# Kernel tuning notes

Hardware: AMD Instinct MI355X
Metric: run time of the kernel (lower is better)

The kernel has to match this reference:

```python
import jax, jax.numpy as jnp
import numpy as np

N, E, F, C, H, L, ED = 100000, 1600000, 128, 16, 2, 2, 4
EPS = 1e-5
NEG_SLOPE = 0.2


def setup_inputs() -> dict:
    key = jax.random.key(0)
    ks = jax.random.split(key, 32)
    s = 0.1
    inp = {
        "x": jax.random.normal(ks[0], (N, F), dtype=jnp.float32),
        "edge_index": jax.random.randint(ks[1], (2, E), 0, N, dtype=jnp.int64),
        "edge_attr": jax.random.uniform(ks[2], (E, ED), dtype=jnp.float32),
        "embed_W": jax.random.normal(ks[3], (F, C)) * s,
        "embed_b": jnp.zeros((C,), jnp.float32),
        "ln0_w": jnp.ones((C,), jnp.float32),
        "ln0_b": jnp.zeros((C,), jnp.float32),
        "Wl": jax.random.normal(ks[4], (L, C, H * C)) * s,
        "bl": jnp.zeros((L, H * C), jnp.float32),
        "Wr": jax.random.normal(ks[5], (L, C, H * C)) * s,
        "br": jnp.zeros((L, H * C), jnp.float32),
        "We": jax.random.normal(ks[6], (L, ED, H * C)) * s,
        "att": jax.random.normal(ks[7], (L, H, C)) * s,
        "gat_b": jnp.zeros((L, H * C), jnp.float32),
        "n1_w": jnp.ones((L, H * C), jnp.float32),
        "n1_b": jnp.zeros((L, H * C), jnp.float32),
        "lin_W": jax.random.normal(ks[8], (L, H * C, C)) * s,
        "lin_b": jnp.zeros((L, C), jnp.float32),
        "n2_w": jnp.ones((L, C), jnp.float32),
        "n2_b": jnp.zeros((L, C), jnp.float32),
    }
    return inp


def _node_ln(v, w, b):
    # torch.nn.LayerNorm over the feature dim (per node)
    mu = v.mean(-1, keepdims=True)
    var = ((v - mu) ** 2).mean(-1, keepdims=True)
    return (v - mu) / jnp.sqrt(var + EPS) * w + b


def _graph_ln(v, w, b):
    # PyG norm.LayerNorm(mode='graph'): normalize over ALL nodes and channels
    mu = v.mean()
    vc = v - mu
    return vc / jnp.sqrt((vc * vc).mean() + EPS) * w + b


def reference(x, edge_index, edge_attr, embed_W, embed_b, ln0_w, ln0_b,
              Wl, bl, Wr, br, We, att, gat_b, n1_w, n1_b,
              lin_W, lin_b, n2_w, n2_b):
    n = x.shape[0]
    heads, c = att.shape[1], att.shape[2]
    layers = Wl.shape[0]

    # node embedding MLP (dropout = identity in eval)
    h = jax.nn.relu(_node_ln(x @ embed_W + embed_b, ln0_w, ln0_b))

    # add self-loops (fill_value=0.0 -> zero edge features, lin_edge has no bias)
    loop = jnp.arange(n)
    src = jnp.concatenate([edge_index[0], loop])
    dst = jnp.concatenate([edge_index[1], loop])

    hs = [h]
    for i in range(layers):
        xl = (h @ Wl[i] + bl[i]).reshape(n, heads, c)   # source transform (x_j)
        xr = (h @ Wr[i] + br[i]).reshape(n, heads, c)   # target transform (x_i)
        ew = (edge_attr @ We[i]).reshape(-1, heads, c)
        ew = jnp.concatenate([ew, jnp.zeros((n, heads, c), ew.dtype)], axis=0)

        msg = xl[src] + xr[dst] + ew                      # [E+N, H, C]
        logits = jnp.einsum('ehc,hc->eh', jax.nn.leaky_relu(msg, NEG_SLOPE), att[i])
        m = jax.ops.segment_max(logits, dst, num_segments=n)
        ex = jnp.exp(logits - m[dst])
        den = jax.ops.segment_sum(ex, dst, num_segments=n)
        alpha = ex / den[dst]                             # segment softmax over dst

        g = jax.ops.segment_sum(alpha[..., None] * xl[src], dst, num_segments=n)
        g = g.reshape(n, heads * c) + gat_b[i]

        g = jax.nn.relu(_graph_ln(g, n1_w[i], n1_b[i]))
        g = g @ lin_W[i] + lin_b[i]
        g = _graph_ln(g, n2_w[i], n2_b[i])
        h = jax.nn.relu(g + h)                            # residual + relu
        hs.append(h)

    # JumpingKnowledge mode='max': elementwise max over layer outputs
    return jnp.max(jnp.stack(hs, axis=0), axis=0)
```

## Files before the change

kernel.cpp:

```cpp
#include <hip/hip_runtime.h>

#define N_NODES 100000
#define N_EDGES 1600000
#define NF 128
#define NC 16
#define NH 2
#define HC 32
#define NL 2
#define NED 4
#define EPS 1e-5f
#define NEG 0.2f
#define NBUCK 196
#define P1_CHUNK 4096
#define P1_BLKS ((N_EDGES + P1_CHUNK - 1) / P1_CHUNK)
#define AGG_BLKS ((N_NODES + 7) / 8)
#define MID_BLKS ((N_NODES + 15) / 16)

__device__ __forceinline__ unsigned short f2bf(float f) {
    unsigned int u = __float_as_uint(f);
    u += 0x7fffu + ((u >> 16) & 1u);
    return (unsigned short)(u >> 16);
}
__device__ __forceinline__ float bf2f(unsigned short u) {
    return __uint_as_float(((unsigned int)u) << 16);
}

__global__ __launch_bounds__(256) void k_embed(
    const float* __restrict__ x, const float* __restrict__ W,
    const float* __restrict__ b, const float* __restrict__ lnw,
    const float* __restrict__ lnb, float* __restrict__ h, float* __restrict__ jk)
{
    __shared__ float Ws[NF * NC];
    __shared__ float xs[16][NF + 4];
    const int t = threadIdx.x;
    for (int i = t; i < NF * NC; i += 256) Ws[i] = W[i];
    const int n0 = blockIdx.x * 16;
    for (int i = t; i < 16 * NF; i += 256) {
        int r = i >> 7, f = i & (NF - 1);
        int n = n0 + r;
        xs[r][f] = (n < N_NODES) ? x[(size_t)n * NF + f] : 0.f;
    }
    __syncthreads();
    const int r = t >> 4;
    const int c = t & 15;
    const int n = n0 + r;
    float acc = b[c];
#pragma unroll 16
    for (int f = 0; f < NF; ++f) acc += xs[r][f] * Ws[f * NC + c];
    float s = acc;
    for (int m = 8; m >= 1; m >>= 1) s += __shfl_xor(s, m, 16);
    float mu = s * (1.f / 16.f);
    float d = acc - mu;
    float v = d * d;
    for (int m = 8; m >= 1; m >>= 1) v += __shfl_xor(v, m, 16);
    float inv = rsqrtf(v * (1.f / 16.f) + EPS);
    float out = fmaxf(d * inv * lnw[c] + lnb[c], 0.f);
    if (n < N_NODES) {
        h[(size_t)n * NC + c]  = out;
        jk[(size_t)n * NC + c] = out;
    }
}

__global__ __launch_bounds__(256) void k_bhist(
    const int* __restrict__ dst, int* __restrict__ bcnt)
{
    __shared__ int hist[256];
    const int t = threadIdx.x;
    hist[t] = 0;
    __syncthreads();
    const int e0 = blockIdx.x * P1_CHUNK;
    const int cnt = min(P1_CHUNK, N_EDGES - e0);
    for (int i = t; i < cnt; i += 256)
        atomicAdd(&hist[dst[e0 + i] >> 9], 1);
    __syncthreads();
    if (hist[t] > 0) atomicAdd(&bcnt[t], hist[t]);
}

__global__ __launch_bounds__(256) void k_bscan(
    const int* __restrict__ bcnt, int* __restrict__ bbase, int* __restrict__ bcur)
{
    __shared__ int tmp[256];
    const int t = threadIdx.x;
    int v0 = bcnt[t];
    tmp[t] = v0;
    __syncthreads();
    for (int off = 1; off < 256; off <<= 1) {
        int v = (t >= off) ? tmp[t - off] : 0;
        __syncthreads();
        tmp[t] += v;
        __syncthreads();
    }
    int excl = tmp[t] - v0;
    bbase[t] = excl;
    bcur[t]  = excl;
    if (t == 255) bbase[256] = tmp[t];
}

__global__ __launch_bounds__(256) void k_pass1(
    const int* __restrict__ src, const int* __restrict__ dst,
    int* __restrict__ bcur, int2* __restrict__ csr_tmp)
{
    __shared__ int2 stage[P1_CHUNK];
    __shared__ unsigned char bstage[P1_CHUNK];
    __shared__ int hist[256];
    __shared__ int exc[256];
    __shared__ int gbase[256];
    __shared__ int scanbuf[256];
    const int t = threadIdx.x;
    const int e0 = blockIdx.x * P1_CHUNK;
    const int cnt = min(P1_CHUNK, N_EDGES - e0);
    hist[t] = 0;
    __syncthreads();
    int mys[16], myb[16], myp[16];
    int nv = 0;
#pragma unroll
    for (int k = 0; k < 16; ++k) {
        int i = k * 256 + t;
        if (i < cnt) {
            int e = e0 + i;
            int d = dst[e];
            mys[nv] = src[e];
            myb[nv] = d >> 9;
            myp[nv] = (e << 9) | (d & 511);
            atomicAdd(&hist[d >> 9], 1);
            ++nv;
        }
    }
    __syncthreads();
    int hv = hist[t];
    scanbuf[t] = hv;
    __syncthreads();
    for (int off = 1; off < 256; off <<= 1) {
        int v = (t >= off) ? scanbuf[t - off] : 0;
        __syncthreads();
        scanbuf[t] += v;
        __syncthreads();
    }
    int ex = scanbuf[t] - hv;
    hist[t] = ex;
    exc[t]  = ex;
    __syncthreads();
    for (int k = 0; k < nv; ++k) {
        int pos = atomicAdd(&hist[myb[k]], 1);
        stage[pos]  = make_int2(mys[k], myp[k]);
        bstage[pos] = (unsigned char)myb[k];
    }
    __syncthreads();
    {
        int c = hist[t] - exc[t];
        gbase[t] = (c > 0) ? atomicAdd(&bcur[t], c) : 0;
    }
    __syncthreads();
    for (int i = t; i < cnt; i += 256) {
        int b = bstage[i];
        csr_tmp[gbase[b] + (i - exc[b])] = stage[i];
    }
}

__global__ __launch_bounds__(256) void k_pass2(
    const int* __restrict__ bbase, const int2* __restrict__ csr_tmp,
    int* __restrict__ offsets, int2* __restrict__ csr_se)
{
    __shared__ int hist[512];
    __shared__ int cur[512];
    __shared__ int scanbuf[256];
    const int b = blockIdx.x, t = threadIdx.x;
    const int ebeg = bbase[b], eend = bbase[b + 1];
    hist[t] = 0; hist[t + 256] = 0;
    __syncthreads();
    for (int i = ebeg + t; i < eend; i += 256)
        atomicAdd(&hist[csr_tmp[i].y & 511], 1);
    __syncthreads();
    int a0 = hist[2 * t], a1 = hist[2 * t + 1];
    int pair = a0 + a1;
    scanbuf[t] = pair;
    __syncthreads();
    for (int off = 1; off < 256; off <<= 1) {
        int v = (t >= off) ? scanbuf[t - off] : 0;
        __syncthreads();
        scanbuf[t] += v;
        __syncthreads();
    }
    int e2 = scanbuf[t] - pair;
    cur[2 * t]     = e2;
    cur[2 * t + 1] = e2 + a0;
    __syncthreads();
    const int n0 = b * 512;
#pragma unroll
    for (int k = 0; k < 2; ++k) {
        int i = t + k * 256;
        int n = n0 + i;
        if (n < N_NODES) offsets[n] = ebeg + cur[i];
    }
    if (b == NBUCK - 1 && t == 0) offsets[N_NODES] = N_EDGES;
    __syncthreads();
    for (int i = ebeg + t; i < eend; i += 256) {
        int2 se = csr_tmp[i];
        int dl = se.y & 511;
        int e  = (int)(((unsigned int)se.y) >> 9);
        int pos = ebeg + atomicAdd(&cur[dl], 1);
        csr_se[pos] = make_int2(se.x, e);
    }
}

__global__ __launch_bounds__(256) void k_trans(
    const float* __restrict__ h, const float* __restrict__ Wl, const float* __restrict__ bl,
    const float* __restrict__ Wr, const float* __restrict__ br,
    unsigned short* __restrict__ xl, unsigned short* __restrict__ xr)
{
    __shared__ float Wls[NC * HC], Wrs[NC * HC];
    __shared__ float hs[8][NC + 1];
    const int t = threadIdx.x;
    for (int i = t; i < NC * HC; i += 256) { Wls[i] = Wl[i]; Wrs[i] = Wr[i]; }
    const int n0 = blockIdx.x * 8;
    for (int i = t; i < 8 * NC; i += 256) {
        int r = i >> 4, c = i & 15;
        int n = n0 + r;
        hs[r][c] = (n < N_NODES) ? h[(size_t)n * NC + c] : 0.f;
    }
    __syncthreads();
    const int r = t >> 5;
    const int j = t & 31;
    const int n = n0 + r;
    float al = bl[j], ar = br[j];
#pragma unroll
    for (int c = 0; c < NC; ++c) {
        float hv = hs[r][c];
        al += hv * Wls[c * HC + j];
        ar += hv * Wrs[c * HC + j];
    }
    if (n < N_NODES) {
        xl[(size_t)n * HC + j] = f2bf(al);
        xr[(size_t)n * HC + j] = f2bf(ar);
    }
}

__device__ __forceinline__ float head_sum(float p) {
    p += __shfl_xor(p, 1, 16);
    p += __shfl_xor(p, 2, 16);
    p += __shfl_xor(p, 4, 16);
    p += __shfl_xor(p, 8, 16);
    return p;
}

__global__ __launch_bounds__(256) void k_agg(
    const int* __restrict__ offsets, const int2* __restrict__ csr_se,
    const float4* __restrict__ ea4,
    const float* __restrict__ We, const float* __restrict__ att,
    const float* __restrict__ gat_b,
    const unsigned short* __restrict__ xl, const unsigned short* __restrict__ xr,
    float* __restrict__ g, float2* __restrict__ part)
{
    __shared__ float Wes[NED * HC];
    __shared__ float atts[HC], gbs[HC];
    const int t = threadIdx.x;
    if (t < NED * HC) Wes[t] = We[t];
    if (t < HC) { atts[t] = att[t]; gbs[t] = gat_b[t]; }
    __syncthreads();
    const int grp = t >> 5;
    const int j   = t & 31;
    const int d = blockIdx.x * 8 + grp;
    float gv = 0.f;
    if (d < N_NODES) {
        const float aj = atts[j];
        const float w0 = Wes[j], w1 = Wes[HC + j], w2 = Wes[2 * HC + j], w3 = Wes[3 * HC + j];
        const float xld = bf2f(xl[(size_t)d * HC + j]);
        const float xrd = bf2f(xr[(size_t)d * HC + j]);
        float m = xld + xrd;
        m = (m > 0.f) ? m : NEG * m;
        float eh = __expf(head_sum(m * aj));
        float acc = eh * xld;
        float den = eh;
        const int base = offsets[d];
        const int deg  = offsets[d + 1] - base;
        int k = 0;
        for (; k + 4 <= deg; k += 4) {
            const int2 s0 = csr_se[base + k];
            const int2 s1 = csr_se[base + k + 1];
            const int2 s2 = csr_se[base + k + 2];
            const int2 s3 = csr_se[base + k + 3];
            const float x0 = bf2f(xl[(size_t)s0.x * HC + j]);
            const float x1 = bf2f(xl[(size_t)s1.x * HC + j]);
            const float x2 = bf2f(xl[(size_t)s2.x * HC + j]);
            const float x3 = bf2f(xl[(size_t)s3.x * HC + j]);
            const float4 e0 = ea4[s0.y];
            const float4 e1 = ea4[s1.y];
            const float4 e2 = ea4[s2.y];
            const float4 e3 = ea4[s3.y];
            float m0 = x0 + xrd + e0.x * w0 + e0.y * w1 + e0.z * w2 + e0.w * w3;
            float m1 = x1 + xrd + e1.x * w0 + e1.y * w1 + e1.z * w2 + e1.w * w3;
            float m2 = x2 + xrd + e2.x * w0 + e2.y * w1 + e2.z * w2 + e2.w * w3;
            float m3 = x3 + xrd + e3.x * w0 + e3.y * w1 + e3.z * w2 + e3.w * w3;
            m0 = (m0 > 0.f) ? m0 : NEG * m0;
            m1 = (m1 > 0.f) ? m1 : NEG * m1;
            m2 = (m2 > 0.f) ? m2 : NEG * m2;
            m3 = (m3 > 0.f) ? m3 : NEG * m3;
            float p0 = m0 * aj, p1 = m1 * aj, p2 = m2 * aj, p3 = m3 * aj;
            p0 += __shfl_xor(p0, 1, 16); p1 += __shfl_xor(p1, 1, 16);
            p2 += __shfl_xor(p2, 1, 16); p3 += __shfl_xor(p3, 1, 16);
            p0 += __shfl_xor(p0, 2, 16); p1 += __shfl_xor(p1, 2, 16);
            p2 += __shfl_xor(p2, 2, 16); p3 += __shfl_xor(p3, 2, 16);
            p0 += __shfl_xor(p0, 4, 16); p1 += __shfl_xor(p1, 4, 16);
            p2 += __shfl_xor(p2, 4, 16); p3 += __shfl_xor(p3, 4, 16);
            p0 += __shfl_xor(p0, 8, 16); p1 += __shfl_xor(p1, 8, 16);
            p2 += __shfl_xor(p2, 8, 16); p3 += __shfl_xor(p3, 8, 16);
            const float ee0 = __expf(p0), ee1 = __expf(p1);
            const float ee2 = __expf(p2), ee3 = __expf(p3);
            acc += ee0 * x0 + ee1 * x1 + ee2 * x2 + ee3 * x3;
            den += ee0 + ee1 + ee2 + ee3;
        }
        for (; k < deg; ++k) {
            const int2 se = csr_se[base + k];
            const float xv = bf2f(xl[(size_t)se.x * HC + j]);
            const float4 ea = ea4[se.y];
            float mm = xv + xrd + ea.x * w0 + ea.y * w1 + ea.z * w2 + ea.w * w3;
            mm = (mm > 0.f) ? mm : NEG * mm;
            const float ee = __expf(head_sum(mm * aj));
            acc += ee * xv;
            den += ee;
        }
        gv = acc / den + gbs[j];
        g[(size_t)d * HC + j] = gv;
    }
    float s = gv, ss = gv * gv;
    for (int m = 32; m >= 1; m >>= 1) { s += __shfl_xor(s, m); ss += __shfl_xor(ss, m); }
    __shared__ float sr[4], ssr[4];
    const int w = t >> 6;
    if ((t & 63) == 0) { sr[w] = s; ssr[w] = ss; }
    __syncthreads();
    if (t == 0) part[blockIdx.x] = make_float2(sr[0] + sr[1] + sr[2] + sr[3],
                                               ssr[0] + ssr[1] + ssr[2] + ssr[3]);
}

__global__ __launch_bounds__(256) void k_red(
    const float2* __restrict__ part, int n, double* __restrict__ out)
{
    const int t = threadIdx.x;
    double s = 0.0, ss = 0.0;
    for (int i = t; i < n; i += 256) {
        float2 p = part[i];
        s += (double)p.x; ss += (double)p.y;
    }
    for (int m = 32; m >= 1; m >>= 1) { s += __shfl_xor(s, m); ss += __shfl_xor(ss, m); }
    __shared__ double sr[4], ssr[4];
    const int w = t >> 6;
    if ((t & 63) == 0) { sr[w] = s; ssr[w] = ss; }
    __syncthreads();
    if (t == 0) {
        out[0] = sr[0] + sr[1] + sr[2] + sr[3];
        out[1] = ssr[0] + ssr[1] + ssr[2] + ssr[3];
    }
}

__global__ __launch_bounds__(256) void k_mid(
    const float* __restrict__ g,
    const float* __restrict__ n1w, const float* __restrict__ n1b,
    const float* __restrict__ linW, const float* __restrict__ linb,
    const double* __restrict__ stats1, float* __restrict__ g2,
    float2* __restrict__ part)
{
    __shared__ float Ws[HC * NC];
    __shared__ float rs[16][HC + 1];
    const int t = threadIdx.x;
    for (int i = t; i < HC * NC; i += 256) Ws[i] = linW[i];
    const double cnt = (double)N_NODES * HC;
    const double mud = stats1[0] / cnt;
    const float mu  = (float)mud;
    const float var = (float)(stats1[1] / cnt - mud * mud);
    const float inv = rsqrtf(var + EPS);
    const int n0 = blockIdx.x * 16;
    for (int i = t; i < 16 * HC; i += 256) {
        int r = i >> 5, j = i & 31;
        int n = n0 + r;
        float v = (n < N_NODES) ? g[(size_t)n * HC + j] : mu;
        v = (v - mu) * inv * n1w[j] + n1b[j];
        rs[r][j] = fmaxf(v, 0.f);
    }
    __syncthreads();
    const int r = t >> 4, c = t & 15;
    const int n = n0 + r;
    float acc = linb[c];
#pragma unroll
    for (int j = 0; j < HC; ++j) acc += rs[r][j] * Ws[j * NC + c];
    float val = (n < N_NODES) ? acc : 0.f;
    if (n < N_NODES) g2[(size_t)n * NC + c] = acc;
    float s = val, ss = val * val;
    for (int m = 32; m >= 1; m >>= 1) { s += __shfl_xor(s, m); ss += __shfl_xor(ss, m); }
    __shared__ float sr[4], ssr[4];
    const int w = t >> 6;
    if ((t & 63) == 0) { sr[w] = s; ssr[w] = ss; }
    __syncthreads();
    if (t == 0) part[blockIdx.x] = make_float2(sr[0] + sr[1] + sr[2] + sr[3],
                                               ssr[0] + ssr[1] + ssr[2] + ssr[3]);
}

__global__ __launch_bounds__(256) void k_final(
    const float* __restrict__ g2, const float* __restrict__ n2w,
    const float* __restrict__ n2b, const double* __restrict__ stats2,
    float* __restrict__ h, float* __restrict__ jk)
{
    const int i = blockIdx.x * 256 + threadIdx.x;
    if (i >= N_NODES * NC) return;
    const double cnt = (double)N_NODES * NC;
    const double mud = stats2[0] / cnt;
    const float mu  = (float)mud;
    const float var = (float)(stats2[1] / cnt - mud * mud);
    const float inv = rsqrtf(var + EPS);
    const int c = i & (NC - 1);
    float v = (g2[i] - mu) * inv * n2w[c] + n2b[c];
    float hn = fmaxf(v + h[i], 0.f);
    h[i] = hn;
    jk[i] = fmaxf(jk[i], hn);
}

extern "C" void kernel_launch(void* const* d_in, const int* in_sizes, int n_in,
                              void* d_out, int out_size, void* d_ws, size_t ws_size,
                              hipStream_t stream)
{
    const float* x     = (const float*)d_in[0];
    const int*   eidx  = (const int*)d_in[1];
    const float* eattr = (const float*)d_in[2];
    const float* embW  = (const float*)d_in[3];
    const float* embB  = (const float*)d_in[4];
    const float* ln0w  = (const float*)d_in[5];
    const float* ln0b  = (const float*)d_in[6];
    const float* Wl    = (const float*)d_in[7];
    const float* bl    = (const float*)d_in[8];
    const float* Wr    = (const float*)d_in[9];
    const float* br    = (const float*)d_in[10];
    const float* We    = (const float*)d_in[11];
    const float* att   = (const float*)d_in[12];
    const float* gatb  = (const float*)d_in[13];
    const float* n1w   = (const float*)d_in[14];
    const float* n1b   = (const float*)d_in[15];
    const float* linW  = (const float*)d_in[16];
    const float* linb  = (const float*)d_in[17];
    const float* n2w   = (const float*)d_in[18];
    const float* n2b   = (const float*)d_in[19];
    float* out = (float*)d_out;

    char* ws = (char*)d_ws;
    double* stats = (double*)ws;
    char* p = ws + 1024;
    int* bcnt  = (int*)p;  p += 1024;
    int* bbase = (int*)p;  p += 2048;
    int* bcur  = (int*)p;  p += 1024;
    int* offsets = (int*)p; p += (size_t)(N_NODES + 64) * 4;
    int2* csr_tmp = (int2*)p; p += (size_t)N_EDGES * 8;
    int2* csr_se  = (int2*)p; p += (size_t)N_EDGES * 8;
    float* h  = (float*)p;   p += (size_t)N_NODES * NC * 4;
    unsigned short* xl = (unsigned short*)p; p += (size_t)N_NODES * HC * 2;
    unsigned short* xr = (unsigned short*)p; p += (size_t)N_NODES * HC * 2;
    float* g   = (float*)p;  p += (size_t)N_NODES * HC * 4;
    float* g2  = (float*)p;  p += (size_t)N_NODES * NC * 4;
    float2* part1 = (float2*)p; p += (size_t)AGG_BLKS * 8;
    float2* part2 = (float2*)p; p += (size_t)MID_BLKS * 8;

    const int* srcp = eidx;
    const int* dstp = eidx + N_EDGES;

    hipMemsetAsync(bcnt, 0, 1024, stream);
    k_bhist<<<P1_BLKS, 256, 0, stream>>>(dstp, bcnt);
    k_bscan<<<1, 256, 0, stream>>>(bcnt, bbase, bcur);
    k_pass1<<<P1_BLKS, 256, 0, stream>>>(srcp, dstp, bcur, csr_tmp);
    k_pass2<<<NBUCK, 256, 0, stream>>>(bbase, csr_tmp, offsets, csr_se);

    k_embed<<<(N_NODES + 15) / 16, 256, 0, stream>>>(x, embW, embB, ln0w, ln0b, h, out);

    for (int l = 0; l < NL; ++l) {
        k_trans<<<(N_NODES + 7) / 8, 256, 0, stream>>>(
            h, Wl + l * NC * HC, bl + l * HC, Wr + l * NC * HC, br + l * HC, xl, xr);
        k_agg<<<AGG_BLKS, 256, 0, stream>>>(
            offsets, csr_se, (const float4*)eattr, We + l * NED * HC, att + l * HC,
            gatb + l * HC, xl, xr, g, part1);
        k_red<<<1, 256, 0, stream>>>(part1, AGG_BLKS, stats);
        k_mid<<<MID_BLKS, 256, 0, stream>>>(
            g, n1w + l * HC, n1b + l * HC,
            linW + l * HC * NC, linb + l * NC, stats, g2, part2);
        k_red<<<1, 256, 0, stream>>>(part2, MID_BLKS, stats + 2);
        k_final<<<(N_NODES * NC + 255) / 256, 256, 0, stream>>>(
            g2, n2w + l * NC, n2b + l * NC, stats + 2, h, out);
    }
}
```

Before: 516.3 us.

## Permute edge attributes into CSR order and fuse reductions via last-block pattern

```diff
diff --git a/kernel.cpp b/kernel.cpp
--- a/kernel.cpp
+++ b/kernel.cpp
@@ -62,9 +62,11 @@
 }
 
 __global__ __launch_bounds__(256) void k_bhist(
-    const int* __restrict__ dst, int* __restrict__ bcnt)
+    const int* __restrict__ dst, int* __restrict__ bcnt, unsigned* __restrict__ ctr,
+    int* __restrict__ bbase, int* __restrict__ bcur)
 {
     __shared__ int hist[256];
+    __shared__ bool amLast;
     const int t = threadIdx.x;
     hist[t] = 0;
     __syncthreads();
@@ -74,31 +76,35 @@
         atomicAdd(&hist[dst[e0 + i] >> 9], 1);
     __syncthreads();
     if (hist[t] > 0) atomicAdd(&bcnt[t], hist[t]);
-}
-
-__global__ __launch_bounds__(256) void k_bscan(
-    const int* __restrict__ bcnt, int* __restrict__ bbase, int* __restrict__ bcur)
-{
-    __shared__ int tmp[256];
-    const int t = threadIdx.x;
-    int v0 = bcnt[t];
-    tmp[t] = v0;
-    __syncthreads();
-    for (int off = 1; off < 256; off <<= 1) {
-        int v = (t >= off) ? tmp[t - off] : 0;
-        __syncthreads();
-        tmp[t] += v;
-        __syncthreads();
-    }
-    int excl = tmp[t] - v0;
-    bbase[t] = excl;
-    bcur[t]  = excl;
-    if (t == 255) bbase[256] = tmp[t];
+    __syncthreads();
+    if (t == 0) {
+        __threadfence();
+        amLast = (atomicAdd(ctr, 1u) == (unsigned)gridDim.x - 1u);
+    }
+    __syncthreads();
+    if (amLast) {
+        __threadfence();
+        int v0 = ((volatile int*)bcnt)[t];
+        __shared__ int tmp[256];
+        tmp[t] = v0;
+        __syncthreads();
+        for (int off = 1; off < 256; off <<= 1) {
+            int v = (t >= off) ? tmp[t - off] : 0;
+            __syncthreads();
+            tmp[t] += v;
+            __syncthreads();
+        }
+        int excl = tmp[t] - v0;
+        bbase[t] = excl;
+        bcur[t]  = excl;
+        if (t == 255) bbase[256] = tmp[t];
+    }
 }
 
 __global__ __launch_bounds__(256) void k_pass1(
     const int* __restrict__ src, const int* __restrict__ dst,
-    int* __restrict__ bcur, int2* __restrict__ csr_tmp)
+    const float4* __restrict__ ea4, int* __restrict__ bcur,
+    int2* __restrict__ tmp_se, float4* __restrict__ tmp_ea)
 {
     __shared__ int2 stage[P1_CHUNK];
     __shared__ unsigned char bstage[P1_CHUNK];
@@ -153,13 +159,18 @@
     __syncthreads();
     for (int i = t; i < cnt; i += 256) {
         int b = bstage[i];
-        csr_tmp[gbase[b] + (i - exc[b])] = stage[i];
+        int2 se = stage[i];
+        int e = (int)(((unsigned int)se.y) >> 9);
+        int gpos = gbase[b] + (i - exc[b]);
+        tmp_se[gpos] = se;
+        tmp_ea[gpos] = ea4[e];
     }
 }
 
 __global__ __launch_bounds__(256) void k_pass2(
-    const int* __restrict__ bbase, const int2* __restrict__ csr_tmp,
-    int* __restrict__ offsets, int2* __restrict__ csr_se)
+    const int* __restrict__ bbase, const int2* __restrict__ tmp_se,
+    const float4* __restrict__ tmp_ea,
+    int* __restrict__ offsets, int* __restrict__ csr_src, float4* __restrict__ csr_ea)
 {
     __shared__ int hist[512];
     __shared__ int cur[512];
@@ -169,7 +180,7 @@
     hist[t] = 0; hist[t + 256] = 0;
     __syncthreads();
     for (int i = ebeg + t; i < eend; i += 256)
-        atomicAdd(&hist[csr_tmp[i].y & 511], 1);
+        atomicAdd(&hist[tmp_se[i].y & 511], 1);
     __syncthreads();
     int a0 = hist[2 * t], a1 = hist[2 * t + 1];
     int pair = a0 + a1;
@@ -181,9 +192,9 @@
         scanbuf[t] += v;
         __syncthreads();
     }
-    int e2 = scanbuf[t] - pair;
-    cur[2 * t]     = e2;
-    cur[2 * t + 1] = e2 + a0;
+    int ex2 = scanbuf[t] - pair;
+    cur[2 * t]     = ex2;
+    cur[2 * t + 1] = ex2 + a0;
     __syncthreads();
     const int n0 = b * 512;
 #pragma unroll
@@ -195,11 +206,12 @@
     if (b == NBUCK - 1 && t == 0) offsets[N_NODES] = N_EDGES;
     __syncthreads();
     for (int i = ebeg + t; i < eend; i += 256) {
-        int2 se = csr_tmp[i];
+        int2 se = tmp_se[i];
+        float4 ea = tmp_ea[i];
         int dl = se.y & 511;
-        int e  = (int)(((unsigned int)se.y) >> 9);
         int pos = ebeg + atomicAdd(&cur[dl], 1);
-        csr_se[pos] = make_int2(se.x, e);
+        csr_src[pos] = se.x;
+        csr_ea[pos]  = ea;
     }
 }
 
@@ -244,15 +256,17 @@
 }
 
 __global__ __launch_bounds__(256) void k_agg(
-    const int* __restrict__ offsets, const int2* __restrict__ csr_se,
-    const float4* __restrict__ ea4,
+    const int* __restrict__ offsets, const int* __restrict__ csr_src,
+    const float4* __restrict__ csr_ea,
     const float* __restrict__ We, const float* __restrict__ att,
     const float* __restrict__ gat_b,
     const unsigned short* __restrict__ xl, const unsigned short* __restrict__ xr,
-    float* __restrict__ g, float2* __restrict__ part)
+    float* __restrict__ g, float2* __restrict__ part,
+    unsigned* __restrict__ ctr, double* __restrict__ stats)
 {
     __shared__ float Wes[NED * HC];
     __shared__ float atts[HC], gbs[HC];
+    __shared__ bool amLast;
     const int t = threadIdx.x;
     if (t < NED * HC) Wes[t] = We[t];
     if (t < HC) { atts[t] = att[t]; gbs[t] = gat_b[t]; }
@@ -275,18 +289,15 @@
         const int deg  = offsets[d + 1] - base;
         int k = 0;
         for (; k + 4 <= deg; k += 4) {
-            const int2 s0 = csr_se[base + k];
-            const int2 s1 = csr_se[base + k + 1];
-            const int2 s2 = csr_se[base + k + 2];
-            const int2 s3 = csr_se[base + k + 3];
-            const float x0 = bf2f(xl[(size_t)s0.x * HC + j]);
-            const float x1 = bf2f(xl[(size_t)s1.x * HC + j]);
-            const float x2 = bf2f(xl[(size_t)s2.x * HC + j]);
-            const float x3 = bf2f(xl[(size_t)s3.x * HC + j]);
-            const float4 e0 = ea4[s0.y];
-            const float4 e1 = ea4[s1.y];
-            const float4 e2 = ea4[s2.y];
-            const float4 e3 = ea4[s3.y];
+            const int b0 = base + k;
+            const int s0 = csr_src[b0],     s1 = csr_src[b0 + 1];
+            const int s2 = csr_src[b0 + 2], s3 = csr_src[b0 + 3];
+            const float4 e0 = csr_ea[b0],     e1 = csr_ea[b0 + 1];
+            const float4 e2 = csr_ea[b0 + 2], e3 = csr_ea[b0 + 3];
+            const float x0 = bf2f(xl[(size_t)s0 * HC + j]);
+            const float x1 = bf2f(xl[(size_t)s1 * HC + j]);
+            const float x2 = bf2f(xl[(size_t)s2 * HC + j]);
+            const float x3 = bf2f(xl[(size_t)s3 * HC + j]);
             float m0 = x0 + xrd + e0.x * w0 + e0.y * w1 + e0.z * w2 + e0.w * w3;
             float m1 = x1 + xrd + e1.x * w0 + e1.y * w1 + e1.z * w2 + e1.w * w3;
             float m2 = x2 + xrd + e2.x * w0 + e2.y * w1 + e2.z * w2 + e2.w * w3;
@@ -310,9 +321,9 @@
             den += ee0 + ee1 + ee2 + ee3;
         }
         for (; k < deg; ++k) {
-            const int2 se = csr_se[base + k];
-            const float xv = bf2f(xl[(size_t)se.x * HC + j]);
-            const float4 ea = ea4[se.y];
+            const int s = csr_src[base + k];
+            const float4 ea = csr_ea[base + k];
+            const float xv = bf2f(xl[(size_t)s * HC + j]);
             float mm = xv + xrd + ea.x * w0 + ea.y * w1 + ea.z * w2 + ea.w * w3;
             mm = (mm > 0.f) ? mm : NEG * mm;
             const float ee = __expf(head_sum(mm * aj));
@@ -328,27 +339,29 @@
     const int w = t >> 6;
     if ((t & 63) == 0) { sr[w] = s; ssr[w] = ss; }
     __syncthreads();
-    if (t == 0) part[blockIdx.x] = make_float2(sr[0] + sr[1] + sr[2] + sr[3],
-                                               ssr[0] + ssr[1] + ssr[2] + ssr[3]);
-}
-
-__global__ __launch_bounds__(256) void k_red(
-    const float2* __restrict__ part, int n, double* __restrict__ out)
-{
-    const int t = threadIdx.x;
-    double s = 0.0, ss = 0.0;
-    for (int i = t; i < n; i += 256) {
-        float2 p = part[i];
-        s += (double)p.x; ss += (double)p.y;
-    }
-    for (int m = 32; m >= 1; m >>= 1) { s += __shfl_xor(s, m); ss += __shfl_xor(ss, m); }
-    __shared__ double sr[4], ssr[4];
-    const int w = t >> 6;
-    if ((t & 63) == 0) { sr[w] = s; ssr[w] = ss; }
-    __syncthreads();
     if (t == 0) {
-        out[0] = sr[0] + sr[1] + sr[2] + sr[3];
-        out[1] = ssr[0] + ssr[1] + ssr[2] + ssr[3];
+        part[blockIdx.x] = make_float2(sr[0] + sr[1] + sr[2] + sr[3],
+                                       ssr[0] + ssr[1] + ssr[2] + ssr[3]);
+        __threadfence();
+        amLast = (atomicAdd(ctr, 1u) == (unsigned)gridDim.x - 1u);
+    }
+    __syncthreads();
+    if (amLast) {
+        __threadfence();
+        double ds = 0.0, dss = 0.0;
+        const volatile float* vp = (const volatile float*)part;
+        for (int i = t; i < (int)gridDim.x; i += 256) {
+            ds  += (double)vp[2 * i];
+            dss += (double)vp[2 * i + 1];
+        }
+        for (int m = 32; m >= 1; m >>= 1) { ds += __shfl_xor(ds, m); dss += __shfl_xor(dss, m); }
+        __shared__ double dsr[4], dssr[4];
+        if ((t & 63) == 0) { dsr[w] = ds; dssr[w] = dss; }
+        __syncthreads();
+        if (t == 0) {
+            stats[0] = dsr[0] + dsr[1] + dsr[2] + dsr[3];
+            stats[1] = dssr[0] + dssr[1] + dssr[2] + dssr[3];
+        }
     }
 }
 
@@ -357,10 +370,12 @@
     const float* __restrict__ n1w, const float* __restrict__ n1b,
     const float* __restrict__ linW, const float* __restrict__ linb,
     const double* __restrict__ stats1, float* __restrict__ g2,
-    float2* __restrict__ part)
+    float2* __restrict__ part, unsigned* __restrict__ ctr,
+    double* __restrict__ stats2)
 {
     __shared__ float Ws[HC * NC];
     __shared__ float rs[16][HC + 1];
+    __shared__ bool amLast;
     const int t = threadIdx.x;
     for (int i = t; i < HC * NC; i += 256) Ws[i] = linW[i];
     const double cnt = (double)N_NODES * HC;
@@ -390,8 +405,77 @@
     const int w = t >> 6;
     if ((t & 63) == 0) { sr[w] = s; ssr[w] = ss; }
     __syncthreads();
-    if (t == 0) part[blockIdx.x] = make_float2(sr[0] + sr[1] + sr[2] + sr[3],
-                                               ssr[0] + ssr[1] + ssr[2] + ssr[3]);
+    if (t == 0) {
+        part[blockIdx.x] = make_float2(sr[0] + sr[1] + sr[2] + sr[3],
+                                       ssr[0] + ssr[1] + ssr[2] + ssr[3]);
+        __threadfence();
+        amLast = (atomicAdd(ctr, 1u) == (unsigned)gridDim.x - 1u);
+    }
+    __syncthreads();
+    if (amLast) {
+        __threadfence();
+        double ds = 0.0, dss = 0.0;
+        const volatile float* vp = (const volatile float*)part;
+        for (int i = t; i < (int)gridDim.x; i += 256) {
+            ds  += (double)vp[2 * i];
+            dss += (double)vp[2 * i + 1];
+        }
+        for (int m = 32; m >= 1; m >>= 1) { ds += __shfl_xor(ds, m); dss += __shfl_xor(dss, m); }
+        __shared__ double dsr[4], dssr[4];
+        if ((t & 63) == 0) { dsr[w] = ds; dssr[w] = dss; }
+        __syncthreads();
+        if (t == 0) {
+            stats2[0] = dsr[0] + dsr[1] + dsr[2] + dsr[3];
+            stats2[1] = dssr[0] + dssr[1] + dssr[2] + dssr[3];
+        }
+    }
+}
+
+__global__ __launch_bounds__(256) void k_ftrans(
+    const float* __restrict__ g2, const float* __restrict__ n2w,
+    const float* __restrict__ n2b, const double* __restrict__ stats2,
+    float* __restrict__ h, float* __restrict__ jk,
+    const float* __restrict__ Wl, const float* __restrict__ bl,
+    const float* __restrict__ Wr, const float* __restrict__ br,
+    unsigned short* __restrict__ xl, unsigned short* __restrict__ xr)
+{
+    __shared__ float Wls[NC * HC], Wrs[NC * HC];
+    __shared__ float hs[8][NC + 1];
+    const int t = threadIdx.x;
+    for (int i = t; i < NC * HC; i += 256) { Wls[i] = Wl[i]; Wrs[i] = Wr[i]; }
+    const double cnt = (double)N_NODES * NC;
+    const double mud = stats2[0] / cnt;
+    const float mu  = (float)mud;
+    const float var = (float)(stats2[1] / cnt - mud * mud);
+    const float inv = rsqrtf(var + EPS);
+    const int n0 = blockIdx.x * 8;
+    if (t < 8 * NC) {
+        int r = t >> 4, c = t & 15;
+        int n = n0 + r;
+        if (n < N_NODES) {
+            size_t idx = (size_t)n * NC + c;
+            float v = (g2[idx] - mu) * inv * n2w[c] + n2b[c];
+            float hn = fmaxf(v + h[idx], 0.f);
+            h[idx] = hn;
+            jk[idx] = fmaxf(jk[idx], hn);
+            hs[r][c] = hn;
+        } else hs[r][c] = 0.f;
+    }
+    __syncthreads();
+    const int r = t >> 5;
+    const int j = t & 31;
+    const int n = n0 + r;
+    float al = bl[j], ar = br[j];
+#pragma unroll
+    for (int c = 0; c < NC; ++c) {
+        float hv = hs[r][c];
+        al += hv * Wls[c * HC + j];
+        ar += hv * Wrs[c * HC + j];
+    }
+    if (n < N_NODES) {
+        xl[(size_t)n * HC + j] = f2bf(al);
+        xr[(size_t)n * HC + j] = f2bf(ar);
+    }
 }
 
 __global__ __launch_bounds__(256) void k_final(
@@ -442,43 +526,56 @@
     char* ws = (char*)d_ws;
     double* stats = (double*)ws;
     char* p = ws + 1024;
-    int* bcnt  = (int*)p;  p += 1024;
-    int* bbase = (int*)p;  p += 2048;
-    int* bcur  = (int*)p;  p += 1024;
+    int* bcnt = (int*)p;
+    unsigned* ctr = (unsigned*)(p + 1024);
+    p += 2048;
+    int* bbase = (int*)p; p += 4096;
+    int* bcur  = (int*)p; p += 1024;
     int* offsets = (int*)p; p += (size_t)(N_NODES + 64) * 4;
-    int2* csr_tmp = (int2*)p; p += (size_t)N_EDGES * 8;
-    int2* csr_se  = (int2*)p; p += (size_t)N_EDGES * 8;
-    float* h  = (float*)p;   p += (size_t)N_NODES * NC * 4;
-    unsigned short* xl = (unsigned short*)p; p += (size_t)N_NODES * HC * 2;
-    unsigned short* xr = (unsigned short*)p; p += (size_t)N_NODES * HC * 2;
-    float* g   = (float*)p;  p += (size_t)N_NODES * HC * 4;
-    float* g2  = (float*)p;  p += (size_t)N_NODES * NC * 4;
-    float2* part1 = (float2*)p; p += (size_t)AGG_BLKS * 8;
-    float2* part2 = (float2*)p; p += (size_t)MID_BLKS * 8;
-
-    const int* srcp = eidx;
-    const int* dstp = eidx + N_EDGES;
-
-    hipMemsetAsync(bcnt, 0, 1024, stream);
-    k_bhist<<<P1_BLKS, 256, 0, stream>>>(dstp, bcnt);
-    k_bscan<<<1, 256, 0, stream>>>(bcnt, bbase, bcur);
-    k_pass1<<<P1_BLKS, 256, 0, stream>>>(srcp, dstp, bcur, csr_tmp);
-    k_pass2<<<NBUCK, 256, 0, stream>>>(bbase, csr_tmp, offsets, csr_se);
-
-    k_embed<<<(N_NODES + 15) / 16, 256, 0, stream>>>(x, embW, embB, ln0w, ln0b, h, out);
-
-    for (int l = 0; l < NL; ++l) {
+    int2* tmp_se = (int2*)p;
+    float* g     = (float*)p;
+    p += (size_t)N_EDGES * 8;
+    int* csr_src = (int*)p; p += (size_t)N_EDGES * 4;
+    float4* csr_ea = (float4*)p; p += (size_t)N_EDGES * 16;
+    float4* tmp_ea = (float4*)p;
+    {
+        char* q = p;
+        p += (size_t)N_EDGES * 16;
+        float* hq = (float*)q; q += (size_t)N_NODES * NC * 4;
+        unsigned short* xlq = (unsigned short*)q; q += (size_t)N_NODES * HC * 2;
+        unsigned short* xrq = (unsigned short*)q; q += (size_t)N_NODES * HC * 2;
+        float* g2q = (float*)q;
+        float2* part1 = (float2*)p; p += (size_t)AGG_BLKS * 8;
+        float2* part2 = (float2*)p; p += (size_t)MID_BLKS * 8;
+
+        const int* srcp = eidx;
+        const int* dstp = eidx + N_EDGES;
+
+        hipMemsetAsync(bcnt, 0, 2048, stream);
+        k_bhist<<<P1_BLKS, 256, 0, stream>>>(dstp, bcnt, ctr, bbase, bcur);
+        k_pass1<<<P1_BLKS, 256, 0, stream>>>(srcp, dstp, (const float4*)eattr,
+                                             bcur, tmp_se, tmp_ea);
+        k_pass2<<<NBUCK, 256, 0, stream>>>(bbase, tmp_se, tmp_ea,
+                                           offsets, csr_src, csr_ea);
+
+        k_embed<<<(N_NODES + 15) / 16, 256, 0, stream>>>(x, embW, embB, ln0w, ln0b, hq, out);
+
         k_trans<<<(N_NODES + 7) / 8, 256, 0, stream>>>(
-            h, Wl + l * NC * HC, bl + l * HC, Wr + l * NC * HC, br + l * HC, xl, xr);
+            hq, Wl, bl, Wr, br, xlq, xrq);
         k_agg<<<AGG_BLKS, 256, 0, stream>>>(
-            offsets, csr_se, (const float4*)eattr, We + l * NED * HC, att + l * HC,
-            gatb + l * HC, xl, xr, g, part1);
-        k_red<<<1, 256, 0, stream>>>(part1, AGG_BLKS, stats);
+            offsets, csr_src, csr_ea, We, att, gatb, xlq, xrq, g, part1, ctr + 1, stats);
         k_mid<<<MID_BLKS, 256, 0, stream>>>(
-            g, n1w + l * HC, n1b + l * HC,
-            linW + l * HC * NC, linb + l * NC, stats, g2, part2);
-        k_red<<<1, 256, 0, stream>>>(part2, MID_BLKS, stats + 2);
+            g, n1w, n1b, linW, linb, stats, g2q, part2, ctr + 2, stats + 2);
+        k_ftrans<<<(N_NODES + 7) / 8, 256, 0, stream>>>(
+            g2q, n2w, n2b, stats + 2, hq, out,
+            Wl + NC * HC, bl + HC, Wr + NC * HC, br + HC, xlq, xrq);
+        k_agg<<<AGG_BLKS, 256, 0, stream>>>(
+            offsets, csr_src, csr_ea, We + NED * HC, att + HC, gatb + HC,
+            xlq, xrq, g, part1, ctr + 3, stats);
+        k_mid<<<MID_BLKS, 256, 0, stream>>>(
+            g, n1w + HC, n1b + HC, linW + HC * NC, linb + NC, stats, g2q,
+            part2, ctr + 4, stats + 2);
         k_final<<<(N_NODES * NC + 255) / 256, 256, 0, stream>>>(
-            g2, n2w + l * NC, n2b + l * NC, stats + 2, h, out);
-    }
-}
+            g2q, n2w + NC, n2b + NC, stats + 2, hq, out);
+    }
+}
```

Result: slower. 1.465 ms (+183.8%).
